# Kernel optimization log

Measured on AMD Instinct MI355X. Metric: run time of the kernel, lower is better.

## Reference

```python
import jax, jax.numpy as jnp
import numpy as np

B, N, C = 2, 32768, 512
H, Dh, G = 8, 64, 64          # heads, dim_head, slice_num
Cd = 256                      # context_dim
EPS = 1e-5


def setup_inputs() -> dict:
    key = jax.random.key(0)
    ks = jax.random.split(key, 16)
    lin = lambda k, i, o: jax.random.normal(k, (i, o), jnp.float32) * 0.02
    inner = H * Dh
    return {
        "x": jax.random.normal(ks[0], (B, N, C), jnp.float32),
        "context": jax.random.normal(ks[1], (B, H, G, Cd), jnp.float32),
        "Wx": lin(ks[2], C, inner),   "bx": jnp.zeros((inner,), jnp.float32),
        "Wfx": lin(ks[3], C, inner),  "bfx": jnp.zeros((inner,), jnp.float32),
        "Wslice": lin(ks[4], Dh, G),  "bslice": jnp.zeros((G,), jnp.float32),
        "temperature": jnp.full((1, H, 1, 1), 0.5, jnp.float32),
        "Wq": lin(ks[5], Dh, Dh),  "bq": jnp.zeros((Dh,), jnp.float32),
        "Wk": lin(ks[6], Dh, Dh),  "bk": jnp.zeros((Dh,), jnp.float32),
        "Wv": lin(ks[7], Dh, Dh),  "bv": jnp.zeros((Dh,), jnp.float32),
        "Wcq": lin(ks[8], Dh, Dh), "bcq": jnp.zeros((Dh,), jnp.float32),
        "Wck": lin(ks[9], Cd, Dh), "bck": jnp.zeros((Dh,), jnp.float32),
        "Wcv": lin(ks[10], Cd, Dh), "bcv": jnp.zeros((Dh,), jnp.float32),
        "state_mixing": jnp.zeros((), jnp.float32),
        "Wo": lin(ks[11], inner, C), "bo": jnp.zeros((C,), jnp.float32),
    }


def _sdpa(q, k, v):
    # q: (b,h,s,d), k/v: (b,h,t,d)
    s = jnp.einsum("bhqd,bhkd->bhqk", q, k) / jnp.sqrt(jnp.asarray(q.shape[-1], q.dtype))
    return jnp.einsum("bhqk,bhkd->bhqd", jax.nn.softmax(s, axis=-1), v)


def reference(x, context, Wx, bx, Wfx, bfx, Wslice, bslice, temperature,
              Wq, bq, Wk, bk, Wv, bv, Wcq, bcq, Wck, bck, Wcv, bcv,
              state_mixing, Wo, bo):
    b, n, _ = x.shape
    # project onto slices: (B,N,C) -> (B,H,N,Dh)
    x_mid = (x @ Wx + bx).reshape(b, n, H, Dh).transpose(0, 2, 1, 3)
    fx_mid = (x @ Wfx + bfx).reshape(b, n, H, Dh).transpose(0, 2, 1, 3)
    # slice weights: (B,H,N,G) with learnable temperature (clamped)
    logits = (x_mid @ Wslice + bslice) / jnp.clip(temperature, 0.1, 5.0)
    w = jax.nn.softmax(logits, axis=-1)
    norm = w.sum(axis=2)  # (B,H,G)
    tokens = jnp.einsum("bhnc,bhng->bhgc", fx_mid, w) / (norm[..., None] + EPS)
    # self-attention over slice tokens
    sa = _sdpa(tokens @ Wq + bq, tokens @ Wk + bk, tokens @ Wv + bv)
    # cross-attention to context
    ca = _sdpa(tokens @ Wcq + bcq, context @ Wck + bck, context @ Wcv + bcv)
    # sigmoid-gated state mixing
    g = jax.nn.sigmoid(state_mixing)
    out_tok = g * sa + (1.0 - g) * ca
    # de-slice back to tokens and output projection
    out_x = jnp.einsum("bhgc,bhng->bhnc", out_tok, w)
    out_x = out_x.transpose(0, 2, 1, 3).reshape(b, n, H * Dh)
    return out_x @ Wo + bo
```

## Files before the change

### kernel.cpp

```cpp
#include <hip/hip_runtime.h>
#include <hip/hip_bf16.h>
#include <cstdint>

typedef __bf16 bf16;
typedef bf16 bf16x8 __attribute__((ext_vector_type(8)));
typedef float floatx4 __attribute__((ext_vector_type(4)));

#define EPS_F 1e-5f

__device__ __forceinline__ void async16(const bf16* g, bf16* l)
{
  __builtin_amdgcn_global_load_lds(
      (const __attribute__((address_space(1))) void*)g,
      (__attribute__((address_space(3))) void*)l, 16, 0, 0);
}

__global__ void k_prep(const float* __restrict__ x, bf16* __restrict__ xb,
                       const float* __restrict__ Wx, const float* __restrict__ bx,
                       const float* __restrict__ Wfx, const float* __restrict__ bfx,
                       const float* __restrict__ Wslice, const float* __restrict__ bslice,
                       const float* __restrict__ temp,
                       bf16* __restrict__ WcatT, float* __restrict__ bcat,
                       float* __restrict__ zbase)
{
  __shared__ float sW[64];
  int bb = blockIdx.x;
  int t = threadIdx.x;
  if (bb < 16384) {
    long i = ((long)bb * 256 + t) * 8;
    floatx4 a = *reinterpret_cast<const floatx4*>(x + i);
    floatx4 b = *reinterpret_cast<const floatx4*>(x + i + 4);
    bf16x8 o;
    #pragma unroll
    for (int e = 0; e < 4; ++e) { o[e] = (bf16)a[e]; o[4 + e] = (bf16)b[e]; }
    *reinterpret_cast<bf16x8*>(xb + i) = o;
  } else if (bb < 17408) {
    int j = bb - 16384;
    if (j < 512) {
      for (int c = t; c < 512; c += 256)
        WcatT[(size_t)j * 512 + c] = (bf16)Wfx[(size_t)c * 512 + j];
      if (t == 0) bcat[j] = bfx[j];
    } else {
      int jj = j - 512;
      int h = jj >> 6, g = jj & 63;
      if (t < 64) sW[t] = Wslice[t * 64 + g];
      __syncthreads();
      float tv = temp[h];
      tv = fminf(fmaxf(tv, 0.1f), 5.0f);
      float invt = 1.0f / tv;
      for (int c = t; c < 512; c += 256) {
        const float* wrow = Wx + (size_t)c * 512 + h * 64;
        float acc = 0.f;
        #pragma unroll
        for (int d = 0; d < 64; ++d) acc += wrow[d] * sW[d];
        WcatT[(size_t)j * 512 + c] = (bf16)(acc * invt);
      }
      if (t == 0) {
        float acc = 0.f;
        for (int d = 0; d < 64; ++d) acc += bx[h * 64 + d] * sW[d];
        bcat[j] = (acc + bslice[g]) * invt;
      }
    }
  } else {
    int z = bb - 17408;
    floatx4 zf = {0.f, 0.f, 0.f, 0.f};
    *reinterpret_cast<floatx4*>(&zbase[((long)z * 256 + t) * 4]) = zf;
  }
}

template <typename OutT, bool SM>
__global__ __launch_bounds__(256, 2) void k_gemm(
    const bf16* __restrict__ A, const bf16* __restrict__ BT,
    OutT* __restrict__ C, const float* __restrict__ bias,
    long Abatch, long Bbatch, long Cbatch, int lda, int ldc, int grid_n)
{
  __shared__ bf16 As[128 * 64];
  __shared__ bf16 Bs[128 * 64];
  const int t = threadIdx.x;
  const int lane = t & 63;
  const int wave = t >> 6;
  const int wm = wave >> 1, wn = wave & 1;
  const int zb = blockIdx.z;
  const bf16* Ab = A + (long)zb * Abatch;
  const bf16* Bb = BT + (long)zb * Bbatch;
  OutT* Cb = C + (long)zb * Cbatch;

  const int L = blockIdx.x;
  const int cx = L & 7;
  const int nb = (L >> 3) % grid_n;
  const int chunk = L / (8 * grid_n);
  const int M0 = (chunk * 8 + cx) * 128;
  const int N0 = nb * 128;

  const int lm = lane & 15;
  const int quad = lane >> 4;
  const int srow = lane >> 3;
  const int sc8 = lane & 7;

  floatx4 acc[4][4] = {};

  for (int kt = 0; kt < 8; ++kt) {
    const int k0 = kt * 64;
    const bf16* gA = Ab + (long)(M0 + wave * 32 + srow) * lda + k0 + sc8 * 8;
    const bf16* gB = Bb + (long)(N0 + wave * 32 + srow) * 512 + k0 + sc8 * 8;
    bf16* lA = &As[wave * 2048];
    bf16* lB = &Bs[wave * 2048];
    #pragma unroll
    for (int i = 0; i < 4; ++i) {
      async16(gA + (long)i * 8 * lda, lA + i * 512);
      async16(gB + (long)i * 8 * 512, lB + i * 512);
    }
    __syncthreads();
    #pragma unroll
    for (int s = 0; s < 2; ++s) {
      const int kl = s * 32 + quad * 8;
      bf16x8 af[4], bfr[4];
      #pragma unroll
      for (int i = 0; i < 4; ++i)
        af[i] = *reinterpret_cast<const bf16x8*>(&As[(wm * 64 + i * 16 + lm) * 64 + kl]);
      #pragma unroll
      for (int j = 0; j < 4; ++j)
        bfr[j] = *reinterpret_cast<const bf16x8*>(&Bs[(wn * 64 + j * 16 + lm) * 64 + kl]);
      #pragma unroll
      for (int i = 0; i < 4; ++i)
        #pragma unroll
        for (int j = 0; j < 4; ++j)
          acc[i][j] = __builtin_amdgcn_mfma_f32_16x16x32_bf16(af[i], bfr[j], acc[i][j], 0, 0, 0);
    }
    __syncthreads();
  }

  float bv[4];
  #pragma unroll
  for (int j = 0; j < 4; ++j) bv[j] = bias[N0 + wn * 64 + j * 16 + lm];

  if (SM && N0 >= 512) {
    #pragma unroll
    for (int i = 0; i < 4; ++i) {
      #pragma unroll
      for (int r = 0; r < 4; ++r) {
        float v[4];
        #pragma unroll
        for (int j = 0; j < 4; ++j) v[j] = acc[i][j][r] + bv[j];
        float m = fmaxf(fmaxf(v[0], v[1]), fmaxf(v[2], v[3]));
        m = fmaxf(m, __shfl_xor(m, 1));
        m = fmaxf(m, __shfl_xor(m, 2));
        m = fmaxf(m, __shfl_xor(m, 4));
        m = fmaxf(m, __shfl_xor(m, 8));
        float e[4], s = 0.f;
        #pragma unroll
        for (int j = 0; j < 4; ++j) { e[j] = __expf(v[j] - m); s += e[j]; }
        s += __shfl_xor(s, 1);
        s += __shfl_xor(s, 2);
        s += __shfl_xor(s, 4);
        s += __shfl_xor(s, 8);
        float inv = 1.0f / s;
        const long gr = M0 + wm * 64 + i * 16 + quad * 4 + r;
        #pragma unroll
        for (int j = 0; j < 4; ++j)
          Cb[gr * ldc + N0 + wn * 64 + j * 16 + lm] = (OutT)(e[j] * inv);
      }
    }
  } else {
    #pragma unroll
    for (int i = 0; i < 4; ++i) {
      const int gr0 = M0 + wm * 64 + i * 16 + quad * 4;
      #pragma unroll
      for (int j = 0; j < 4; ++j) {
        const int gc = N0 + wn * 64 + j * 16 + lm;
        #pragma unroll
        for (int r = 0; r < 4; ++r)
          Cb[(long)(gr0 + r) * ldc + gc] = (OutT)(acc[i][j][r] + bv[j]);
      }
    }
  }
}

__global__ __launch_bounds__(256) void k_tokens(const bf16* __restrict__ mid,
                                                float* __restrict__ raw,
                                                float* __restrict__ norm)
{
  __shared__ float wt[64][72];
  __shared__ float ft[64][72];
  int kc = blockIdx.x;
  int bh = blockIdx.y;
  int b = bh >> 3, h = bh & 7;
  long rbase = (long)b * 32768 + (long)kc * 1024;
  int t = threadIdx.x;
  int lrow = t >> 2, seg = t & 3;
  int tg = t >> 4, tc = t & 15;
  float acc[4][4] = {};
  float na[4] = {0.f, 0.f, 0.f, 0.f};
  for (int sub = 0; sub < 16; ++sub) {
    long r0 = rbase + sub * 64 + lrow;
    const bf16* fsrc = mid + r0 * 1024 + h * 64 + seg * 16;
    const bf16* wsrc = mid + r0 * 1024 + 512 + h * 64 + seg * 16;
    bf16x8 w0 = *(const bf16x8*)wsrc, w1 = *(const bf16x8*)(wsrc + 8);
    bf16x8 f0 = *(const bf16x8*)fsrc, f1 = *(const bf16x8*)(fsrc + 8);
    #pragma unroll
    for (int e = 0; e < 8; ++e) {
      wt[lrow][seg * 16 + e] = (float)w0[e];
      wt[lrow][seg * 16 + 8 + e] = (float)w1[e];
      ft[lrow][seg * 16 + e] = (float)f0[e];
      ft[lrow][seg * 16 + 8 + e] = (float)f1[e];
    }
    __syncthreads();
    #pragma unroll 4
    for (int n = 0; n < 64; ++n) {
      floatx4 wv = *(const floatx4*)&wt[n][tg * 4];
      floatx4 fv = *(const floatx4*)&ft[n][tc * 4];
      #pragma unroll
      for (int gi = 0; gi < 4; ++gi)
        #pragma unroll
        for (int ci = 0; ci < 4; ++ci) acc[gi][ci] += wv[gi] * fv[ci];
      if (tc == 0) {
        #pragma unroll
        for (int gi = 0; gi < 4; ++gi) na[gi] += wv[gi];
      }
    }
    __syncthreads();
  }
  float* rb = raw + (size_t)bh * 4096;
  #pragma unroll
  for (int gi = 0; gi < 4; ++gi)
    #pragma unroll
    for (int ci = 0; ci < 4; ++ci)
      atomicAdd(&rb[(tg * 4 + gi) * 64 + tc * 4 + ci], acc[gi][ci]);
  if (tc == 0) {
    #pragma unroll
    for (int gi = 0; gi < 4; ++gi) atomicAdd(&norm[bh * 64 + tg * 4 + gi], na[gi]);
  }
}

__global__ __launch_bounds__(256) void k_ctx(const float* __restrict__ ctx,
                                             const float* __restrict__ Wck, const float* __restrict__ bck,
                                             const float* __restrict__ Wcv, const float* __restrict__ bcv,
                                             float* __restrict__ ckbuf, float* __restrict__ cvbuf)
{
  __shared__ float sW[256 * 64];
  int bh = blockIdx.x;
  int which = blockIdx.y;
  const float* W = which ? Wcv : Wck;
  const float* bb = which ? bcv : bck;
  float* outp = which ? cvbuf : ckbuf;
  int t = threadIdx.x;
  for (int i = t; i < 4096; i += 256)
    *(floatx4*)&sW[i * 4] = *(const floatx4*)(W + i * 4);
  __syncthreads();
  int r = t >> 2, c0 = (t & 3) * 16;
  const float* crow = ctx + ((size_t)bh * 64 + r) * 256;
  float acc[16] = {};
  for (int e4 = 0; e4 < 64; ++e4) {
    floatx4 cvv = *(const floatx4*)(crow + e4 * 4);
    #pragma unroll
    for (int ee = 0; ee < 4; ++ee) {
      float cval = cvv[ee];
      int e = e4 * 4 + ee;
      #pragma unroll
      for (int q = 0; q < 4; ++q) {
        floatx4 w4 = *(const floatx4*)&sW[e * 64 + c0 + q * 4];
        acc[q * 4 + 0] += cval * w4[0];
        acc[q * 4 + 1] += cval * w4[1];
        acc[q * 4 + 2] += cval * w4[2];
        acc[q * 4 + 3] += cval * w4[3];
      }
    }
  }
  size_t base = (size_t)bh * 4096 + r * 64 + c0;
  #pragma unroll
  for (int i = 0; i < 16; ++i) outp[base + i] = acc[i] + bb[c0 + i];
}

__global__ __launch_bounds__(256) void k_attn(
    const float* __restrict__ raw, const float* __restrict__ norm,
    const float* __restrict__ Wq, const float* __restrict__ bq,
    const float* __restrict__ Wk, const float* __restrict__ bk,
    const float* __restrict__ Wv, const float* __restrict__ bv,
    const float* __restrict__ Wcq, const float* __restrict__ bcq,
    const float* __restrict__ ck, const float* __restrict__ cv,
    const float* __restrict__ smix, float* __restrict__ ot)
{
  __shared__ float T0[4096];
  __shared__ float T1[4096];
  __shared__ float T2[4096];
  __shared__ float T3[4096];
  int bh = blockIdx.x;
  int t = threadIdx.x;
  int r = t >> 2;
  int c0 = (t & 3) * 16;
  size_t base = (size_t)bh * 4096;

  float invn = 1.0f / (norm[bh * 64 + r] + EPS_F);
  #pragma unroll
  for (int i = 0; i < 16; ++i)
    T0[r * 64 + c0 + i] = raw[base + r * 64 + c0 + i] * invn;
  __syncthreads();

  float acq[16] = {};
  {
    float aq[16] = {}, ak[16] = {}, av[16] = {};
    for (int d = 0; d < 64; ++d) {
      float x = T0[r * 64 + d];
      #pragma unroll
      for (int q = 0; q < 4; ++q) {
        floatx4 wq = *(const floatx4*)(Wq + d * 64 + c0 + q * 4);
        floatx4 wk = *(const floatx4*)(Wk + d * 64 + c0 + q * 4);
        floatx4 wv = *(const floatx4*)(Wv + d * 64 + c0 + q * 4);
        floatx4 wc = *(const floatx4*)(Wcq + d * 64 + c0 + q * 4);
        #pragma unroll
        for (int e = 0; e < 4; ++e) {
          aq[q * 4 + e] += x * wq[e];
          ak[q * 4 + e] += x * wk[e];
          av[q * 4 + e] += x * wv[e];
          acq[q * 4 + e] += x * wc[e];
        }
      }
    }
    __syncthreads();
    #pragma unroll
    for (int i = 0; i < 16; ++i) {
      T1[r * 64 + c0 + i] = aq[i] + bq[c0 + i];
      T2[r * 64 + c0 + i] = ak[i] + bk[c0 + i];
      T3[r * 64 + c0 + i] = av[i] + bv[c0 + i];
      acq[i] += bcq[c0 + i];
    }
  }
  __syncthreads();

  {
    float p[16];
    float mx = -1e30f;
    #pragma unroll
    for (int i = 0; i < 16; ++i) {
      int cc = c0 + i;
      float s = 0.f;
      #pragma unroll
      for (int d4 = 0; d4 < 16; ++d4) {
        floatx4 qv = *(const floatx4*)&T1[r * 64 + d4 * 4];
        floatx4 kv = *(const floatx4*)&T2[cc * 64 + d4 * 4];
        s += qv[0] * kv[0] + qv[1] * kv[1] + qv[2] * kv[2] + qv[3] * kv[3];
      }
      p[i] = s * 0.125f;
      mx = fmaxf(mx, p[i]);
    }
    mx = fmaxf(mx, __shfl_xor(mx, 1));
    mx = fmaxf(mx, __shfl_xor(mx, 2));
    float sum = 0.f;
    #pragma unroll
    for (int i = 0; i < 16; ++i) { p[i] = __expf(p[i] - mx); sum += p[i]; }
    sum += __shfl_xor(sum, 1);
    sum += __shfl_xor(sum, 2);
    float inv = 1.0f / sum;
    #pragma unroll
    for (int i = 0; i < 16; ++i) T0[r * 64 + c0 + i] = p[i] * inv;
  }
  __syncthreads();

  float sa[16] = {};
  for (int g = 0; g < 64; ++g) {
    float pv = T0[r * 64 + g];
    #pragma unroll
    for (int i4 = 0; i4 < 4; ++i4) {
      floatx4 vv = *(const floatx4*)&T3[g * 64 + c0 + i4 * 4];
      sa[i4 * 4 + 0] += pv * vv[0];
      sa[i4 * 4 + 1] += pv * vv[1];
      sa[i4 * 4 + 2] += pv * vv[2];
      sa[i4 * 4 + 3] += pv * vv[3];
    }
  }
  __syncthreads();

  #pragma unroll
  for (int i = 0; i < 16; ++i) {
    T3[r * 64 + c0 + i] = acq[i];
    T1[r * 64 + c0 + i] = ck[base + r * 64 + c0 + i];
    T2[r * 64 + c0 + i] = cv[base + r * 64 + c0 + i];
  }
  __syncthreads();

  {
    float p[16];
    float mx = -1e30f;
    #pragma unroll
    for (int i = 0; i < 16; ++i) {
      int cc = c0 + i;
      float s = 0.f;
      #pragma unroll
      for (int d4 = 0; d4 < 16; ++d4) {
        floatx4 qv = *(const floatx4*)&T3[r * 64 + d4 * 4];
        floatx4 kv = *(const floatx4*)&T1[cc * 64 + d4 * 4];
        s += qv[0] * kv[0] + qv[1] * kv[1] + qv[2] * kv[2] + qv[3] * kv[3];
      }
      p[i] = s * 0.125f;
      mx = fmaxf(mx, p[i]);
    }
    mx = fmaxf(mx, __shfl_xor(mx, 1));
    mx = fmaxf(mx, __shfl_xor(mx, 2));
    float sum = 0.f;
    #pragma unroll
    for (int i = 0; i < 16; ++i) { p[i] = __expf(p[i] - mx); sum += p[i]; }
    sum += __shfl_xor(sum, 1);
    sum += __shfl_xor(sum, 2);
    float inv = 1.0f / sum;
    #pragma unroll
    for (int i = 0; i < 16; ++i) T0[r * 64 + c0 + i] = p[i] * inv;
  }
  __syncthreads();

  float ca[16] = {};
  for (int g = 0; g < 64; ++g) {
    float pv = T0[r * 64 + g];
    #pragma unroll
    for (int i4 = 0; i4 < 4; ++i4) {
      floatx4 vv = *(const floatx4*)&T2[g * 64 + c0 + i4 * 4];
      ca[i4 * 4 + 0] += pv * vv[0];
      ca[i4 * 4 + 1] += pv * vv[1];
      ca[i4 * 4 + 2] += pv * vv[2];
      ca[i4 * 4 + 3] += pv * vv[3];
    }
  }
  float gmix = 1.0f / (1.0f + __expf(-smix[0]));
  #pragma unroll
  for (int i = 0; i < 16; ++i)
    ot[base + r * 64 + c0 + i] = gmix * sa[i] + (1.0f - gmix) * ca[i];
}

__global__ __launch_bounds__(256) void k_mcat(const float* __restrict__ ot,
                                              const float* __restrict__ Wo,
                                              bf16* __restrict__ McatT)
{
  __shared__ float woS[64][68];
  __shared__ float otS[64][68];
  int jt = blockIdx.x;
  int b = blockIdx.y;
  int t = threadIdx.x;
  int jl = t >> 2;
  int s4 = t & 3;
  int srow = t >> 2, sc = t & 3;
  for (int h = 0; h < 8; ++h) {
    {
      const float* src = Wo + (size_t)(h * 64 + srow) * 512 + jt * 64 + sc * 16;
      #pragma unroll
      for (int q = 0; q < 4; ++q)
        *reinterpret_cast<floatx4*>(&woS[srow][sc * 16 + q * 4]) =
            *reinterpret_cast<const floatx4*>(src + q * 4);
    }
    {
      const float* src = ot + ((size_t)(b * 8 + h)) * 4096 + srow * 64 + sc * 16;
      #pragma unroll
      for (int q = 0; q < 4; ++q)
        *reinterpret_cast<floatx4*>(&otS[srow][sc * 16 + q * 4]) =
            *reinterpret_cast<const floatx4*>(src + q * 4);
    }
    __syncthreads();
    float wcol[64];
    #pragma unroll
    for (int c = 0; c < 64; ++c) wcol[c] = woS[c][jl];
    #pragma unroll
    for (int g = 0; g < 16; ++g) {
      int gg = s4 * 16 + g;
      float a = 0.f;
      #pragma unroll
      for (int c = 0; c < 64; ++c) a += otS[gg][c] * wcol[c];
      McatT[((size_t)b * 512 + (size_t)jt * 64 + jl) * 512 + h * 64 + gg] = (bf16)a;
    }
    __syncthreads();
  }
}

extern "C" void kernel_launch(void* const* d_in, const int* in_sizes, int n_in,
                              void* d_out, int out_size, void* d_ws, size_t ws_size,
                              hipStream_t stream)
{
  const float* x      = (const float*)d_in[0];
  const float* contxt = (const float*)d_in[1];
  const float* Wx     = (const float*)d_in[2];
  const float* bx     = (const float*)d_in[3];
  const float* Wfx    = (const float*)d_in[4];
  const float* bfx    = (const float*)d_in[5];
  const float* Wslice = (const float*)d_in[6];
  const float* bslice = (const float*)d_in[7];
  const float* temp   = (const float*)d_in[8];
  const float* Wq  = (const float*)d_in[9];  const float* bq  = (const float*)d_in[10];
  const float* Wk  = (const float*)d_in[11]; const float* bk  = (const float*)d_in[12];
  const float* Wv  = (const float*)d_in[13]; const float* bv  = (const float*)d_in[14];
  const float* Wcq = (const float*)d_in[15]; const float* bcq = (const float*)d_in[16];
  const float* Wck = (const float*)d_in[17]; const float* bck = (const float*)d_in[18];
  const float* Wcv = (const float*)d_in[19]; const float* bcv = (const float*)d_in[20];
  const float* smix = (const float*)d_in[21];
  const float* Wo = (const float*)d_in[22];  const float* bo = (const float*)d_in[23];
  float* out = (float*)d_out;

  char* ws = (char*)d_ws;
  bf16*  midbuf = (bf16*)(ws + 0);
  bf16*  xb     = (bf16*)(ws + 134217728);
  bf16*  WcatT  = (bf16*)(ws + 201326592);
  bf16*  McatT  = (bf16*)(ws + 202375168);
  float* bcat   = (float*)(ws + 203423744);
  float* traw   = (float*)(ws + 203427840);
  float* norm   = (float*)(ws + 203689984);
  float* otbuf  = (float*)(ws + 203694080);
  float* ckbuf  = (float*)(ws + 203956224);
  float* cvbuf  = (float*)(ws + 204218368);

  k_prep<<<dim3(17473), 256, 0, stream>>>(x, xb, Wx, bx, Wfx, bfx, Wslice, bslice,
                                          temp, WcatT, bcat, traw);

  k_gemm<bf16, true><<<dim3(4096, 1, 1), 256, 0, stream>>>(
      xb, WcatT, midbuf, bcat, 0, 0, 0, 512, 1024, 8);

  k_tokens<<<dim3(32, 16), 256, 0, stream>>>(midbuf, traw, norm);

  k_ctx<<<dim3(16, 2), 256, 0, stream>>>(contxt, Wck, bck, Wcv, bcv, ckbuf, cvbuf);

  k_attn<<<dim3(16), 256, 0, stream>>>(traw, norm, Wq, bq, Wk, bk, Wv, bv, Wcq, bcq,
                                       ckbuf, cvbuf, smix, otbuf);

  k_mcat<<<dim3(8, 2), 256, 0, stream>>>(otbuf, Wo, McatT);

  k_gemm<float, false><<<dim3(1024, 1, 2), 256, 0, stream>>>(
      midbuf + 512, McatT, out, bo,
      (long)32768 * 1024, (long)512 * 512, (long)32768 * 512, 1024, 512, 4);
}
```

Baseline: 750.7 us.

## Fold context projection into prep, split attention paths and parallelize mcat

Moves the context K/V projection into the prep kernel as extra blocks, which removes one launch. The attention kernel now runs the self-attention and cross-attention paths as separate blocks (grid 16x2), and the gated mixing moves into the mcat kernel, which now runs one block per (batch, head, column tile) instead of looping over heads. The goal is to cut serial latency in the small token-stage kernels, which previously ran on only 16 blocks. In exchange it adds an extra intermediate buffer and more global traffic between stages, and the context projection now reads its weights from global memory rather than LDS.

```diff
diff --git a/kernel.cpp b/kernel.cpp
--- a/kernel.cpp
+++ b/kernel.cpp
@@ -21,7 +21,11 @@
                        const float* __restrict__ Wslice, const float* __restrict__ bslice,
                        const float* __restrict__ temp,
                        bf16* __restrict__ WcatT, float* __restrict__ bcat,
-                       float* __restrict__ zbase)
+                       float* __restrict__ zbase,
+                       const float* __restrict__ ctx,
+                       const float* __restrict__ Wck, const float* __restrict__ bck,
+                       const float* __restrict__ Wcv, const float* __restrict__ bcv,
+                       float* __restrict__ ckbuf, float* __restrict__ cvbuf)
 {
   __shared__ float sW[64];
   int bb = blockIdx.x;
@@ -61,10 +65,38 @@
         bcat[j] = (acc + bslice[g]) * invt;
       }
     }
-  } else {
+  } else if (bb < 17473) {
     int z = bb - 17408;
     floatx4 zf = {0.f, 0.f, 0.f, 0.f};
     *reinterpret_cast<floatx4*>(&zbase[((long)z * 256 + t) * 4]) = zf;
+  } else {
+    int z = bb - 17473;
+    int bh = z >> 1, which = z & 1;
+    const float* W = which ? Wcv : Wck;
+    const float* bvec = which ? bcv : bck;
+    float* outp = which ? cvbuf : ckbuf;
+    int r = t >> 2, c0 = (t & 3) * 16;
+    const float* crow = ctx + ((size_t)bh * 64 + r) * 256;
+    float acc[16] = {};
+    for (int e4 = 0; e4 < 64; ++e4) {
+      floatx4 cvv = *(const floatx4*)(crow + e4 * 4);
+      #pragma unroll
+      for (int ee = 0; ee < 4; ++ee) {
+        float cval = cvv[ee];
+        int e = e4 * 4 + ee;
+        #pragma unroll
+        for (int q = 0; q < 4; ++q) {
+          floatx4 w4 = *(const floatx4*)(W + e * 64 + c0 + q * 4);
+          acc[q * 4 + 0] += cval * w4[0];
+          acc[q * 4 + 1] += cval * w4[1];
+          acc[q * 4 + 2] += cval * w4[2];
+          acc[q * 4 + 3] += cval * w4[3];
+        }
+      }
+    }
+    size_t ob = (size_t)bh * 4096 + r * 64 + c0;
+    #pragma unroll
+    for (int i = 0; i < 16; ++i) outp[ob + i] = acc[i] + bvec[c0 + i];
   }
 }
 
@@ -232,59 +264,21 @@
   }
 }
 
-__global__ __launch_bounds__(256) void k_ctx(const float* __restrict__ ctx,
-                                             const float* __restrict__ Wck, const float* __restrict__ bck,
-                                             const float* __restrict__ Wcv, const float* __restrict__ bcv,
-                                             float* __restrict__ ckbuf, float* __restrict__ cvbuf)
-{
-  __shared__ float sW[256 * 64];
-  int bh = blockIdx.x;
-  int which = blockIdx.y;
-  const float* W = which ? Wcv : Wck;
-  const float* bb = which ? bcv : bck;
-  float* outp = which ? cvbuf : ckbuf;
-  int t = threadIdx.x;
-  for (int i = t; i < 4096; i += 256)
-    *(floatx4*)&sW[i * 4] = *(const floatx4*)(W + i * 4);
-  __syncthreads();
-  int r = t >> 2, c0 = (t & 3) * 16;
-  const float* crow = ctx + ((size_t)bh * 64 + r) * 256;
-  float acc[16] = {};
-  for (int e4 = 0; e4 < 64; ++e4) {
-    floatx4 cvv = *(const floatx4*)(crow + e4 * 4);
-    #pragma unroll
-    for (int ee = 0; ee < 4; ++ee) {
-      float cval = cvv[ee];
-      int e = e4 * 4 + ee;
-      #pragma unroll
-      for (int q = 0; q < 4; ++q) {
-        floatx4 w4 = *(const floatx4*)&sW[e * 64 + c0 + q * 4];
-        acc[q * 4 + 0] += cval * w4[0];
-        acc[q * 4 + 1] += cval * w4[1];
-        acc[q * 4 + 2] += cval * w4[2];
-        acc[q * 4 + 3] += cval * w4[3];
-      }
-    }
-  }
-  size_t base = (size_t)bh * 4096 + r * 64 + c0;
-  #pragma unroll
-  for (int i = 0; i < 16; ++i) outp[base + i] = acc[i] + bb[c0 + i];
-}
-
-__global__ __launch_bounds__(256) void k_attn(
+__global__ __launch_bounds__(256) void k_attn2(
     const float* __restrict__ raw, const float* __restrict__ norm,
     const float* __restrict__ Wq, const float* __restrict__ bq,
     const float* __restrict__ Wk, const float* __restrict__ bk,
     const float* __restrict__ Wv, const float* __restrict__ bv,
     const float* __restrict__ Wcq, const float* __restrict__ bcq,
     const float* __restrict__ ck, const float* __restrict__ cv,
-    const float* __restrict__ smix, float* __restrict__ ot)
+    float* __restrict__ sabuf, float* __restrict__ cabuf)
 {
   __shared__ float T0[4096];
   __shared__ float T1[4096];
   __shared__ float T2[4096];
   __shared__ float T3[4096];
   int bh = blockIdx.x;
+  int path = blockIdx.y;
   int t = threadIdx.x;
   int r = t >> 2;
   int c0 = (t & 3) * 16;
@@ -294,10 +288,16 @@
   #pragma unroll
   for (int i = 0; i < 16; ++i)
     T0[r * 64 + c0 + i] = raw[base + r * 64 + c0 + i] * invn;
+  if (path == 1) {
+    #pragma unroll
+    for (int i = 0; i < 16; ++i) {
+      T1[r * 64 + c0 + i] = ck[base + r * 64 + c0 + i];
+      T2[r * 64 + c0 + i] = cv[base + r * 64 + c0 + i];
+    }
+  }
   __syncthreads();
 
-  float acq[16] = {};
-  {
+  if (path == 0) {
     float aq[16] = {}, ak[16] = {}, av[16] = {};
     for (int d = 0; d < 64; ++d) {
       float x = T0[r * 64 + d];
@@ -306,28 +306,39 @@
         floatx4 wq = *(const floatx4*)(Wq + d * 64 + c0 + q * 4);
         floatx4 wk = *(const floatx4*)(Wk + d * 64 + c0 + q * 4);
         floatx4 wv = *(const floatx4*)(Wv + d * 64 + c0 + q * 4);
-        floatx4 wc = *(const floatx4*)(Wcq + d * 64 + c0 + q * 4);
         #pragma unroll
         for (int e = 0; e < 4; ++e) {
           aq[q * 4 + e] += x * wq[e];
           ak[q * 4 + e] += x * wk[e];
           av[q * 4 + e] += x * wv[e];
-          acq[q * 4 + e] += x * wc[e];
         }
       }
     }
-    __syncthreads();
     #pragma unroll
     for (int i = 0; i < 16; ++i) {
       T1[r * 64 + c0 + i] = aq[i] + bq[c0 + i];
       T2[r * 64 + c0 + i] = ak[i] + bk[c0 + i];
       T3[r * 64 + c0 + i] = av[i] + bv[c0 + i];
-      acq[i] += bcq[c0 + i];
-    }
+    }
+  } else {
+    float acq[16] = {};
+    for (int d = 0; d < 64; ++d) {
+      float x = T0[r * 64 + d];
+      #pragma unroll
+      for (int q = 0; q < 4; ++q) {
+        floatx4 wc = *(const floatx4*)(Wcq + d * 64 + c0 + q * 4);
+        #pragma unroll
+        for (int e = 0; e < 4; ++e) acq[q * 4 + e] += x * wc[e];
+      }
+    }
+    #pragma unroll
+    for (int i = 0; i < 16; ++i) T3[r * 64 + c0 + i] = acq[i] + bcq[c0 + i];
   }
   __syncthreads();
 
   {
+    const float* Q = (path == 0) ? T1 : T3;
+    const float* K = (path == 0) ? T2 : T1;
     float p[16];
     float mx = -1e30f;
     #pragma unroll
@@ -336,8 +347,8 @@
       float s = 0.f;
       #pragma unroll
       for (int d4 = 0; d4 < 16; ++d4) {
-        floatx4 qv = *(const floatx4*)&T1[r * 64 + d4 * 4];
-        floatx4 kv = *(const floatx4*)&T2[cc * 64 + d4 * 4];
+        floatx4 qv = *(const floatx4*)&Q[r * 64 + d4 * 4];
+        floatx4 kv = *(const floatx4*)&K[cc * 64 + d4 * 4];
         s += qv[0] * kv[0] + qv[1] * kv[1] + qv[2] * kv[2] + qv[3] * kv[3];
       }
       p[i] = s * 0.125f;
@@ -356,116 +367,84 @@
   }
   __syncthreads();
 
-  float sa[16] = {};
-  for (int g = 0; g < 64; ++g) {
-    float pv = T0[r * 64 + g];
-    #pragma unroll
-    for (int i4 = 0; i4 < 4; ++i4) {
-      floatx4 vv = *(const floatx4*)&T3[g * 64 + c0 + i4 * 4];
-      sa[i4 * 4 + 0] += pv * vv[0];
-      sa[i4 * 4 + 1] += pv * vv[1];
-      sa[i4 * 4 + 2] += pv * vv[2];
-      sa[i4 * 4 + 3] += pv * vv[3];
-    }
-  }
-  __syncthreads();
-
-  #pragma unroll
-  for (int i = 0; i < 16; ++i) {
-    T3[r * 64 + c0 + i] = acq[i];
-    T1[r * 64 + c0 + i] = ck[base + r * 64 + c0 + i];
-    T2[r * 64 + c0 + i] = cv[base + r * 64 + c0 + i];
-  }
-  __syncthreads();
-
   {
-    float p[16];
-    float mx = -1e30f;
-    #pragma unroll
-    for (int i = 0; i < 16; ++i) {
-      int cc = c0 + i;
-      float s = 0.f;
-      #pragma unroll
-      for (int d4 = 0; d4 < 16; ++d4) {
-        floatx4 qv = *(const floatx4*)&T3[r * 64 + d4 * 4];
-        floatx4 kv = *(const floatx4*)&T1[cc * 64 + d4 * 4];
-        s += qv[0] * kv[0] + qv[1] * kv[1] + qv[2] * kv[2] + qv[3] * kv[3];
-      }
-      p[i] = s * 0.125f;
-      mx = fmaxf(mx, p[i]);
-    }
-    mx = fmaxf(mx, __shfl_xor(mx, 1));
-    mx = fmaxf(mx, __shfl_xor(mx, 2));
-    float sum = 0.f;
-    #pragma unroll
-    for (int i = 0; i < 16; ++i) { p[i] = __expf(p[i] - mx); sum += p[i]; }
-    sum += __shfl_xor(sum, 1);
-    sum += __shfl_xor(sum, 2);
-    float inv = 1.0f / sum;
-    #pragma unroll
-    for (int i = 0; i < 16; ++i) T0[r * 64 + c0 + i] = p[i] * inv;
-  }
-  __syncthreads();
-
-  float ca[16] = {};
-  for (int g = 0; g < 64; ++g) {
-    float pv = T0[r * 64 + g];
-    #pragma unroll
-    for (int i4 = 0; i4 < 4; ++i4) {
-      floatx4 vv = *(const floatx4*)&T2[g * 64 + c0 + i4 * 4];
-      ca[i4 * 4 + 0] += pv * vv[0];
-      ca[i4 * 4 + 1] += pv * vv[1];
-      ca[i4 * 4 + 2] += pv * vv[2];
-      ca[i4 * 4 + 3] += pv * vv[3];
-    }
-  }
-  float gmix = 1.0f / (1.0f + __expf(-smix[0]));
-  #pragma unroll
-  for (int i = 0; i < 16; ++i)
-    ot[base + r * 64 + c0 + i] = gmix * sa[i] + (1.0f - gmix) * ca[i];
-}
-
-__global__ __launch_bounds__(256) void k_mcat(const float* __restrict__ ot,
-                                              const float* __restrict__ Wo,
-                                              bf16* __restrict__ McatT)
-{
-  __shared__ float woS[64][68];
+    const float* V = (path == 0) ? T3 : T2;
+    float* dst = (path == 0) ? sabuf : cabuf;
+    float oa[16] = {};
+    for (int g = 0; g < 64; ++g) {
+      float pv = T0[r * 64 + g];
+      #pragma unroll
+      for (int i4 = 0; i4 < 4; ++i4) {
+        floatx4 vv = *(const floatx4*)&V[g * 64 + c0 + i4 * 4];
+        oa[i4 * 4 + 0] += pv * vv[0];
+        oa[i4 * 4 + 1] += pv * vv[1];
+        oa[i4 * 4 + 2] += pv * vv[2];
+        oa[i4 * 4 + 3] += pv * vv[3];
+      }
+    }
+    #pragma unroll
+    for (int i = 0; i < 16; ++i) dst[base + r * 64 + c0 + i] = oa[i];
+  }
+}
+
+__global__ __launch_bounds__(256) void k_mcat2(const float* __restrict__ sabuf,
+                                               const float* __restrict__ cabuf,
+                                               const float* __restrict__ smix,
+                                               const float* __restrict__ Wo,
+                                               bf16* __restrict__ McatT)
+{
+  __shared__ float woT[64][68];
   __shared__ float otS[64][68];
   int jt = blockIdx.x;
-  int b = blockIdx.y;
+  int bh = blockIdx.y;
+  int b = bh >> 3, h = bh & 7;
   int t = threadIdx.x;
-  int jl = t >> 2;
-  int s4 = t & 3;
-  int srow = t >> 2, sc = t & 3;
-  for (int h = 0; h < 8; ++h) {
-    {
-      const float* src = Wo + (size_t)(h * 64 + srow) * 512 + jt * 64 + sc * 16;
-      #pragma unroll
-      for (int q = 0; q < 4; ++q)
-        *reinterpret_cast<floatx4*>(&woS[srow][sc * 16 + q * 4]) =
-            *reinterpret_cast<const floatx4*>(src + q * 4);
-    }
-    {
-      const float* src = ot + ((size_t)(b * 8 + h)) * 4096 + srow * 64 + sc * 16;
-      #pragma unroll
-      for (int q = 0; q < 4; ++q)
-        *reinterpret_cast<floatx4*>(&otS[srow][sc * 16 + q * 4]) =
-            *reinterpret_cast<const floatx4*>(src + q * 4);
-    }
-    __syncthreads();
-    float wcol[64];
-    #pragma unroll
-    for (int c = 0; c < 64; ++c) wcol[c] = woS[c][jl];
-    #pragma unroll
-    for (int g = 0; g < 16; ++g) {
-      int gg = s4 * 16 + g;
-      float a = 0.f;
-      #pragma unroll
-      for (int c = 0; c < 64; ++c) a += otS[gg][c] * wcol[c];
-      McatT[((size_t)b * 512 + (size_t)jt * 64 + jl) * 512 + h * 64 + gg] = (bf16)a;
-    }
-    __syncthreads();
-  }
+  float gm = 1.0f / (1.0f + __expf(-smix[0]));
+  int c = t >> 2, sc = t & 3;
+
+  {
+    const float* src = Wo + (size_t)(h * 64 + c) * 512 + jt * 64 + sc * 16;
+    float tmp[16];
+    #pragma unroll
+    for (int q = 0; q < 4; ++q) {
+      floatx4 v = *(const floatx4*)(src + q * 4);
+      tmp[q * 4 + 0] = v[0]; tmp[q * 4 + 1] = v[1];
+      tmp[q * 4 + 2] = v[2]; tmp[q * 4 + 3] = v[3];
+    }
+    #pragma unroll
+    for (int ji = 0; ji < 16; ++ji) woT[sc * 16 + ji][c] = tmp[ji];
+  }
+  {
+    const float* sp = sabuf + (size_t)bh * 4096 + c * 64 + sc * 16;
+    const float* cp = cabuf + (size_t)bh * 4096 + c * 64 + sc * 16;
+    #pragma unroll
+    for (int q = 0; q < 4; ++q) {
+      floatx4 s4 = *(const floatx4*)(sp + q * 4);
+      floatx4 c4 = *(const floatx4*)(cp + q * 4);
+      floatx4 m4;
+      #pragma unroll
+      for (int e = 0; e < 4; ++e) m4[e] = gm * s4[e] + (1.0f - gm) * c4[e];
+      *(floatx4*)&otS[c][sc * 16 + q * 4] = m4;
+    }
+  }
+  __syncthreads();
+
+  int j = t >> 2, g0 = (t & 3) * 16;
+  float acc[16] = {};
+  for (int c4 = 0; c4 < 16; ++c4) {
+    floatx4 wv = *(const floatx4*)&woT[j][c4 * 4];
+    #pragma unroll
+    for (int gi = 0; gi < 16; ++gi) {
+      floatx4 ov = *(const floatx4*)&otS[g0 + gi][c4 * 4];
+      acc[gi] += wv[0] * ov[0] + wv[1] * ov[1] + wv[2] * ov[2] + wv[3] * ov[3];
+    }
+  }
+  size_t row = (size_t)b * 512 + jt * 64 + j;
+  bf16x8 o0, o1;
+  #pragma unroll
+  for (int e = 0; e < 8; ++e) { o0[e] = (bf16)acc[e]; o1[e] = (bf16)acc[8 + e]; }
+  *reinterpret_cast<bf16x8*>(&McatT[row * 512 + h * 64 + g0]) = o0;
+  *reinterpret_cast<bf16x8*>(&McatT[row * 512 + h * 64 + g0 + 8]) = o1;
 }
 
 extern "C" void kernel_launch(void* const* d_in, const int* in_sizes, int n_in,
@@ -499,24 +478,24 @@
   float* bcat   = (float*)(ws + 203423744);
   float* traw   = (float*)(ws + 203427840);
   float* norm   = (float*)(ws + 203689984);
-  float* otbuf  = (float*)(ws + 203694080);
-  float* ckbuf  = (float*)(ws + 203956224);
-  float* cvbuf  = (float*)(ws + 204218368);
-
-  k_prep<<<dim3(17473), 256, 0, stream>>>(x, xb, Wx, bx, Wfx, bfx, Wslice, bslice,
-                                          temp, WcatT, bcat, traw);
+  float* sabuf  = (float*)(ws + 203694080);
+  float* cabuf  = (float*)(ws + 203956224);
+  float* ckbuf  = (float*)(ws + 204218368);
+  float* cvbuf  = (float*)(ws + 204480512);
+
+  k_prep<<<dim3(17505), 256, 0, stream>>>(x, xb, Wx, bx, Wfx, bfx, Wslice, bslice,
+                                          temp, WcatT, bcat, traw,
+                                          contxt, Wck, bck, Wcv, bcv, ckbuf, cvbuf);
 
   k_gemm<bf16, true><<<dim3(4096, 1, 1), 256, 0, stream>>>(
       xb, WcatT, midbuf, bcat, 0, 0, 0, 512, 1024, 8);
 
   k_tokens<<<dim3(32, 16), 256, 0, stream>>>(midbuf, traw, norm);
 
-  k_ctx<<<dim3(16, 2), 256, 0, stream>>>(contxt, Wck, bck, Wcv, bcv, ckbuf, cvbuf);
-
-  k_attn<<<dim3(16), 256, 0, stream>>>(traw, norm, Wq, bq, Wk, bk, Wv, bv, Wcq, bcq,
-                                       ckbuf, cvbuf, smix, otbuf);
-
-  k_mcat<<<dim3(8, 2), 256, 0, stream>>>(otbuf, Wo, McatT);
+  k_attn2<<<dim3(16, 2), 256, 0, stream>>>(traw, norm, Wq, bq, Wk, bk, Wv, bv,
+                                           Wcq, bcq, ckbuf, cvbuf, sabuf, cabuf);
+
+  k_mcat2<<<dim3(8, 16), 256, 0, stream>>>(sabuf, cabuf, smix, Wo, McatT);
 
   k_gemm<float, false><<<dim3(1024, 1, 2), 256, 0, stream>>>(
       midbuf + 512, McatT, out, bo,
```

Measured after the change: 642.6 us. -14.4%, faster.
